# Optimization experiments

Measured on AMD Instinct MI355X. Metric: run time of the kernel, lower is better.

The kernel has to match this reference:

```python
import jax, jax.numpy as jnp
import numpy as np

B, S, H = 2, 8192, 1024
NUM_HEADS = 16
HEAD_DIM = H // NUM_HEADS
KERNEL = 7
DILATION = 1
SCALE = 1.0 / np.sqrt(HEAD_DIM)


def setup_inputs() -> dict:
    key = jax.random.key(0)
    ks = jax.random.split(key, 9)
    init = 0.02
    return {
        "hidden_states": jax.random.normal(ks[0], (B, S, H), dtype=jnp.float32),
        "w_q": jax.random.normal(ks[1], (H, H), dtype=jnp.float32) * init,
        "b_q": jnp.zeros((H,), dtype=jnp.float32),
        "w_k": jax.random.normal(ks[2], (H, H), dtype=jnp.float32) * init,
        "b_k": jnp.zeros((H,), dtype=jnp.float32),
        "w_v": jax.random.normal(ks[3], (H, H), dtype=jnp.float32) * init,
        "b_v": jnp.zeros((H,), dtype=jnp.float32),
        "w_o": jax.random.normal(ks[4], (H, H), dtype=jnp.float32) * init,
        "b_o": jnp.zeros((H,), dtype=jnp.float32),
    }


def reference(hidden_states, w_q, b_q, w_k, b_k, w_v, b_v, w_o, b_o):
    b, s, h = hidden_states.shape
    # QKV projections (weights stored [in, out])
    q = hidden_states @ w_q + b_q
    k = hidden_states @ w_k + b_k
    v = hidden_states @ w_v + b_v
    # [B, nH, S, hd]
    q = q.reshape(b, s, NUM_HEADS, HEAD_DIM).transpose(0, 2, 1, 3)
    k = k.reshape(b, s, NUM_HEADS, HEAD_DIM).transpose(0, 2, 1, 3)
    v = v.reshape(b, s, NUM_HEADS, HEAD_DIM).transpose(0, 2, 1, 3)

    # Neighborhood window indices: for query i, keys at i + (j - K//2)*dilation
    offsets = (jnp.arange(KERNEL) - KERNEL // 2) * DILATION  # [K]
    idx = jnp.arange(s)[:, None] + offsets[None, :]          # [S, K]
    valid = (idx >= 0) & (idx < s)                           # [S, K]
    idx_c = jnp.clip(idx, 0, s - 1)

    k_win = k[:, :, idx_c, :]  # [B, nH, S, K, hd]
    v_win = v[:, :, idx_c, :]  # [B, nH, S, K, hd]

    scores = jnp.einsum('bhsd,bhskd->bhsk', q, k_win) * SCALE
    scores = jnp.where(valid[None, None], scores, -jnp.inf)
    attn = jax.nn.softmax(scores, axis=-1)                   # [B, nH, S, K]
    out = jnp.einsum('bhsk,bhskd->bhsd', attn, v_win)        # [B, nH, S, hd]

    out = out.transpose(0, 2, 1, 3).reshape(b, s, h)
    return out @ w_o + b_o
```

## Files before the change

### kernel.cpp

```cpp
#include <hip/hip_runtime.h>


typedef __bf16 bf16x8 __attribute__((ext_vector_type(8)));
typedef float f32x4 __attribute__((ext_vector_type(4)));
typedef int int4v __attribute__((ext_vector_type(4)));
typedef unsigned short u16x8 __attribute__((ext_vector_type(8)));
typedef __attribute__((address_space(1))) void as1_void;
typedef __attribute__((address_space(3))) void as3_void;

__device__ __forceinline__ float bf2f(unsigned short u) {
    union { unsigned int u; float f; } c;
    c.u = ((unsigned int)u) << 16;
    return c.f;
}
__device__ __forceinline__ unsigned short f2bf(float f) {
    union { float f; unsigned int u; } c;
    c.f = f;
    unsigned int u = c.u;
    u += 0x7fffu + ((u >> 16) & 1u);
    return (unsigned short)(u >> 16);
}

__global__ __launch_bounds__(256) void prep(
    const float* __restrict__ X, const float* __restrict__ w0,
    const float* __restrict__ w1, const float* __restrict__ w2,
    const float* __restrict__ w3, const float* __restrict__ bq,
    const float* __restrict__ bk, const float* __restrict__ bv,
    unsigned short* __restrict__ Xb, unsigned short* __restrict__ t0,
    unsigned short* __restrict__ t3, float* __restrict__ biasQ) {
    __shared__ unsigned short tile[32][33];
    const int bid = blockIdx.x;
    if (bid < 16384) {
        int i = bid * 256 + threadIdx.x;
        float4 v = ((const float4*)X)[i];
        ushort4 o;
        o.x = f2bf(v.x); o.y = f2bf(v.y); o.z = f2bf(v.z); o.w = f2bf(v.w);
        ((ushort4*)Xb)[i] = o;
    } else if (bid < 20480) {
        const int t = bid - 16384;
        const int z = t >> 10;
        const int rem = t & 1023;
        const float* W = (z == 0) ? w0 : (z == 1) ? w1 : (z == 2) ? w2 : w3;
        unsigned short* Wt = (z == 3) ? t3 : t0 + (size_t)z * 1048576;
        const int c0 = (rem & 31) * 32;
        const int r0 = (rem >> 5) * 32;
        const int tx = threadIdx.x & 31;
        const int ty = threadIdx.x >> 5;
#pragma unroll
        for (int i = 0; i < 32; i += 8)
            tile[ty + i][tx] = f2bf(W[(size_t)(r0 + ty + i) * 1024 + c0 + tx]);
        __syncthreads();
#pragma unroll
        for (int i = 0; i < 32; i += 8)
            Wt[(size_t)(c0 + ty + i) * 1024 + r0 + tx] = tile[tx][ty + i];
    } else {
        int i = (bid - 20480) * 256 + threadIdx.x;
        if (i < 3072)
            biasQ[i] = (i < 1024) ? bq[i] : ((i < 2048) ? bk[i - 1024] : bv[i - 2048]);
    }
}

__global__ __launch_bounds__(512, 2) void gemm_qkv8(
    const unsigned short* __restrict__ A, const unsigned short* __restrict__ Bt,
    const float* __restrict__ bias, unsigned short* __restrict__ Cb) {
    constexpr int K = 1024;
    constexpr int NT = 16;
    __shared__ unsigned short smem[65536];
    const int tid  = threadIdx.x;
    const int lane = tid & 63;
    const int wave = tid >> 6;
    const int quad = lane >> 4;
    const int mr   = lane & 15;

    const int id  = blockIdx.x;
    const int swz = (id & 7) * 96 + (id >> 3);
    const int bm  = (swz / 12) * 256;
    const int bn  = (swz % 12) * 256;
    const int wm  = (wave >> 2) * 128;
    const int wn  = (wave & 3) * 64;

    const int r0 = tid >> 3;
    const int g8 = ((lane & 7) ^ ((lane >> 3) & 7)) * 8;
    const unsigned short* srcA = A  + (size_t)(bm + r0) * K + g8;
    const unsigned short* srcB = Bt + (size_t)(bn + r0) * K + g8;

    auto stage = [&](const unsigned short* gb, int ldsByte, int kt) {
#pragma unroll
        for (int l = 0; l < 2; ++l)
            __builtin_amdgcn_global_load_lds(
                (const as1_void*)(gb + (size_t)l * 65536 + kt),
                (as3_void*)((char*)smem + ldsByte + l * 8192 + tid * 16),
                16, 0, 0);
    };

    stage(srcA,          0,     0);
    stage(srcA + 131072, 16384, 0);
    stage(srcB,          32768, 0);
    stage(srcB + 131072, 49152, 0);
    stage(srcB,          65536 + 32768, 64);
    stage(srcB + 131072, 65536 + 49152, 64);
    asm volatile("s_waitcnt vmcnt(4)" ::: "memory");
    asm volatile("s_barrier" ::: "memory");

    const int aRow = (wm + mr) * 64;
    const int bRow = 16384 + (wn + mr) * 64;
    const int c8_0 = ((0 * 4 + quad) ^ (mr & 7)) * 8;
    const int c8_1 = ((1 * 4 + quad) ^ (mr & 7)) * 8;

    f32x4 acc[8][4] = {};

    for (int t = 0; t < NT; ++t) {
        const int bufS  = (t & 1) << 15;
        const int nbufB = ((t + 1) & 1) << 16;
        const int cbufB = (t & 1) << 16;
        const int ktA = (t + 1 < NT ? t + 1 : NT - 1) * 64;
        const int ktB = (t + 2 < NT ? t + 2 : NT - 1) * 64;

        bf16x8 afL[4][2], bA[2][2], bB[2][2];
#pragma unroll
        for (int i = 0; i < 4; ++i) {
            afL[i][0] = *(const bf16x8*)(smem + bufS + aRow + i * 1024 + c8_0);
            afL[i][1] = *(const bf16x8*)(smem + bufS + aRow + i * 1024 + c8_1);
        }
#pragma unroll
        for (int j = 0; j < 2; ++j) {
            bA[j][0] = *(const bf16x8*)(smem + bufS + bRow + j * 1024 + c8_0);
            bA[j][1] = *(const bf16x8*)(smem + bufS + bRow + j * 1024 + c8_1);
        }
#pragma unroll
        for (int j = 0; j < 2; ++j) {
            bB[j][0] = *(const bf16x8*)(smem + bufS + bRow + (j + 2) * 1024 + c8_0);
            bB[j][1] = *(const bf16x8*)(smem + bufS + bRow + (j + 2) * 1024 + c8_1);
        }
        stage(srcA, nbufB, ktA);
        __builtin_amdgcn_s_setprio(1);
#pragma unroll
        for (int i = 0; i < 4; ++i)
#pragma unroll
            for (int j = 0; j < 2; ++j) {
                acc[i][j] = __builtin_amdgcn_mfma_f32_16x16x32_bf16(afL[i][0], bA[j][0], acc[i][j], 0, 0, 0);
                acc[i][j] = __builtin_amdgcn_mfma_f32_16x16x32_bf16(afL[i][1], bA[j][1], acc[i][j], 0, 0, 0);
            }
        __builtin_amdgcn_s_setprio(0);
        asm volatile("s_barrier" ::: "memory");

        stage(srcA + 131072, nbufB + 16384, ktA);
        __builtin_amdgcn_s_setprio(1);
#pragma unroll
        for (int i = 0; i < 4; ++i)
#pragma unroll
            for (int j = 0; j < 2; ++j) {
                acc[i][j + 2] = __builtin_amdgcn_mfma_f32_16x16x32_bf16(afL[i][0], bB[j][0], acc[i][j + 2], 0, 0, 0);
                acc[i][j + 2] = __builtin_amdgcn_mfma_f32_16x16x32_bf16(afL[i][1], bB[j][1], acc[i][j + 2], 0, 0, 0);
            }
        __builtin_amdgcn_s_setprio(0);
        asm volatile("s_barrier" ::: "memory");

        bf16x8 afH[4][2];
#pragma unroll
        for (int i = 0; i < 4; ++i) {
            afH[i][0] = *(const bf16x8*)(smem + bufS + aRow + (i + 4) * 1024 + c8_0);
            afH[i][1] = *(const bf16x8*)(smem + bufS + aRow + (i + 4) * 1024 + c8_1);
        }
        stage(srcB, cbufB + 32768, ktB);
        __builtin_amdgcn_s_setprio(1);
#pragma unroll
        for (int i = 0; i < 4; ++i)
#pragma unroll
            for (int j = 0; j < 2; ++j) {
                acc[i + 4][j + 2] = __builtin_amdgcn_mfma_f32_16x16x32_bf16(afH[i][0], bB[j][0], acc[i + 4][j + 2], 0, 0, 0);
                acc[i + 4][j + 2] = __builtin_amdgcn_mfma_f32_16x16x32_bf16(afH[i][1], bB[j][1], acc[i + 4][j + 2], 0, 0, 0);
            }
        __builtin_amdgcn_s_setprio(0);
        asm volatile("s_barrier" ::: "memory");

        stage(srcB + 131072, cbufB + 49152, ktB);
        __builtin_amdgcn_s_setprio(1);
#pragma unroll
        for (int i = 0; i < 4; ++i)
#pragma unroll
            for (int j = 0; j < 2; ++j) {
                acc[i + 4][j] = __builtin_amdgcn_mfma_f32_16x16x32_bf16(afH[i][0], bA[j][0], acc[i + 4][j], 0, 0, 0);
                acc[i + 4][j] = __builtin_amdgcn_mfma_f32_16x16x32_bf16(afH[i][1], bA[j][1], acc[i + 4][j], 0, 0, 0);
            }
        __builtin_amdgcn_s_setprio(0);
        asm volatile("s_waitcnt vmcnt(4)" ::: "memory");
        asm volatile("s_barrier" ::: "memory");
    }

    asm volatile("s_waitcnt vmcnt(0) lgkmcnt(0)" ::: "memory");
    asm volatile("s_barrier" ::: "memory");

    unsigned short* ep = smem + wave * 8192;
#pragma unroll
    for (int h = 0; h < 2; ++h) {
#pragma unroll
        for (int j = 0; j < 4; ++j) {
            const float bvv = bias[bn + wn + j * 16 + mr];
#pragma unroll
            for (int i = 0; i < 4; ++i)
#pragma unroll
                for (int r = 0; r < 4; ++r)
                    ep[(i * 16 + quad * 4 + r) * 68 + j * 16 + mr] =
                        f2bf(acc[h * 4 + i][j][r] + bvv);
        }
#pragma unroll
        for (int p = 0; p < 8; ++p) {
            const int row = p * 8 + (lane >> 3);
            const int gr = lane & 7;
            int4v v = *(const int4v*)(ep + row * 68 + gr * 8);
            *(int4v*)(Cb + (size_t)(bm + wm + h * 64 + row) * 3072 + bn + wn + gr * 8) = v;
        }
    }
}

__global__ __launch_bounds__(256) void attn_valu(
    const unsigned short* __restrict__ QKV, unsigned short* __restrict__ out) {
    const int tid = threadIdx.x;
    const int h   = tid & 15;
    const int tl  = tid >> 4;
    const int tok = blockIdx.x * 16 + tl;
    const int s   = tok & 8191;
    const size_t base = (size_t)tok * 3072 + h * 64;

    float qf[64];
#pragma unroll
    for (int i = 0; i < 8; ++i) {
        u16x8 qv = *(const u16x8*)(QKV + base + i * 8);
#pragma unroll
        for (int e = 0; e < 8; ++e) qf[i * 8 + e] = bf2f(qv[e]);
    }

    float sc[7];
#pragma unroll
    for (int j = 0; j < 7; ++j) {
        const int ks = s + j - 3;
        const bool ok = (ks >= 0) & (ks < 8192);
        const int kc = ks < 0 ? 0 : (ks > 8191 ? 8191 : ks);
        const size_t kb = base + (size_t)(kc - s) * 3072 + 1024;
        float acc = 0.f;
#pragma unroll
        for (int i = 0; i < 8; ++i) {
            u16x8 kv = *(const u16x8*)(QKV + kb + i * 8);
#pragma unroll
            for (int e = 0; e < 8; ++e) acc += qf[i * 8 + e] * bf2f(kv[e]);
        }
        sc[j] = ok ? acc * 0.125f : -__builtin_inff();
    }

    float mx = sc[0];
#pragma unroll
    for (int j = 1; j < 7; ++j) mx = fmaxf(mx, sc[j]);
    float p[7], sum = 0.f;
#pragma unroll
    for (int j = 0; j < 7; ++j) {
        p[j] = __builtin_amdgcn_exp2f((sc[j] - mx) * 1.44269504f);
        sum += p[j];
    }
    const float inv = __builtin_amdgcn_rcpf(sum);

    float o[64] = {};
#pragma unroll
    for (int j = 0; j < 7; ++j) {
        const int ks = s + j - 3;
        const int kc = ks < 0 ? 0 : (ks > 8191 ? 8191 : ks);
        const size_t vb = base + (size_t)(kc - s) * 3072 + 2048;
        const float pj = p[j] * inv;
#pragma unroll
        for (int i = 0; i < 8; ++i) {
            u16x8 vv = *(const u16x8*)(QKV + vb + i * 8);
#pragma unroll
            for (int e = 0; e < 8; ++e) o[i * 8 + e] += pj * bf2f(vv[e]);
        }
    }

    const size_t dst = (size_t)tok * 1024 + h * 64;
#pragma unroll
    for (int i = 0; i < 8; ++i) {
        u16x8 ov;
#pragma unroll
        for (int e = 0; e < 8; ++e) ov[e] = f2bf(o[i * 8 + e]);
        *(u16x8*)(out + dst + i * 8) = ov;
    }
}

template <int MODE, int MT>
__device__ __forceinline__ void gemm_body(
    const unsigned short* __restrict__ A, const unsigned short* __restrict__ Bt,
    const float* __restrict__ bias, float* __restrict__ Cf,
    int N, int K) {
    __shared__ unsigned short smem[MT * 2048 + 8192];
    const int tid = threadIdx.x;
    const int lane = tid & 63;
    const int wave = tid >> 6;
    const int bm = blockIdx.y * (MT * 32);
    const int bn = blockIdx.x * 128;
    const int wm = (wave >> 1) * (MT * 16);
    const int wn = (wave & 1) * 64;
    const int quad = lane >> 4;
    const int mr = lane & 15;

    const unsigned short* gA[MT];
    const unsigned short* gB[4];
    char* lA[MT];
    char* lB[4];
#pragma unroll
    for (int k = 0; k < MT; ++k) {
        const int q = (k * 4 + wave) * 64 + lane;
        const int row = q >> 3;
        const int c8 = (q & 7) ^ (row & 7);
        gA[k] = A + (size_t)(bm + row) * K + c8 * 8;
        lA[k] = (char*)smem + (size_t)(k * 4 + wave) * 1024;
    }
#pragma unroll
    for (int k = 0; k < 4; ++k) {
        const int q = (k * 4 + wave) * 64 + lane;
        const int row = q >> 3;
        const int c8 = (q & 7) ^ (row & 7);
        gB[k] = Bt + (size_t)(bn + row) * K + c8 * 8;
        lB[k] = (char*)smem + (size_t)MT * 4096 + (size_t)(k * 4 + wave) * 1024;
    }

    f32x4 acc[MT][4] = {};

    for (int kt = 0; kt < K; kt += 64) {
#pragma unroll
        for (int k = 0; k < MT; ++k) {
            __builtin_amdgcn_global_load_lds((as1_void*)gA[k], (as3_void*)lA[k], 16, 0, 0);
            gA[k] += 64;
        }
#pragma unroll
        for (int k = 0; k < 4; ++k) {
            __builtin_amdgcn_global_load_lds((as1_void*)gB[k], (as3_void*)lB[k], 16, 0, 0);
            gB[k] += 64;
        }
        __syncthreads();

#pragma unroll
        for (int kk = 0; kk < 2; ++kk) {
            const int c8 = (kk * 4 + quad) ^ (mr & 7);
            bf16x8 af[MT], bfr[4];
#pragma unroll
            for (int i = 0; i < MT; ++i)
                af[i] = *(const bf16x8*)(smem + (wm + i * 16 + mr) * 64 + c8 * 8);
#pragma unroll
            for (int j = 0; j < 4; ++j)
                bfr[j] = *(const bf16x8*)(smem + MT * 2048 + (wn + j * 16 + mr) * 64 + c8 * 8);
#pragma unroll
            for (int i = 0; i < MT; ++i)
#pragma unroll
                for (int j = 0; j < 4; ++j)
                    acc[i][j] = __builtin_amdgcn_mfma_f32_16x16x32_bf16(
                        af[i], bfr[j], acc[i][j], 0, 0, 0);
        }
        __syncthreads();
    }

    if (MODE == 0) {
        float* epf = (float*)smem + wave * 1280;
#pragma unroll
        for (int j = 0; j < 4; ++j) {
            const int gcol0 = bn + wn + j * 16;
            const float bv = bias[gcol0 + mr];
#pragma unroll
            for (int h2 = 0; h2 < MT / 4; ++h2) {
#pragma unroll
                for (int i2 = 0; i2 < 4; ++i2)
#pragma unroll
                    for (int r = 0; r < 4; ++r)
                        epf[(i2 * 16 + quad * 4 + r) * 20 + mr] = acc[h2 * 4 + i2][j][r] + bv;
#pragma unroll
                for (int p = 0; p < 4; ++p) {
                    const int dr = p * 16 + (lane >> 2);
                    const int ch = lane & 3;
                    f32x4 v = *(const f32x4*)(epf + dr * 20 + ch * 4);
                    *(f32x4*)(Cf + (size_t)(bm + wm + h2 * 64 + dr) * N + gcol0 + ch * 4) = v;
                }
            }
        }
    }
}

__global__ __launch_bounds__(256, 4) void gemm_out(
    const unsigned short* __restrict__ A, const unsigned short* __restrict__ Bt,
    const float* __restrict__ bias, float* __restrict__ Cf, int N, int K) {
    gemm_body<0, 4>(A, Bt, bias, Cf, N, K);
}

extern "C" void kernel_launch(void* const* d_in, const int* in_sizes, int n_in,
                              void* d_out, int out_size, void* d_ws, size_t ws_size,
                              hipStream_t stream) {
    (void)in_sizes; (void)n_in; (void)out_size; (void)ws_size;
    const float* X  = (const float*)d_in[0];
    const float* wq = (const float*)d_in[1];
    const float* bq = (const float*)d_in[2];
    const float* wk = (const float*)d_in[3];
    const float* bk = (const float*)d_in[4];
    const float* wv = (const float*)d_in[5];
    const float* bv = (const float*)d_in[6];
    const float* wo = (const float*)d_in[7];
    const float* bo = (const float*)d_in[8];
    float* out = (float*)d_out;

    char* ws = (char*)d_ws;
    unsigned short* Xb    = (unsigned short*)(ws);
    unsigned short* WtQKV = (unsigned short*)(ws + 33554432);
    unsigned short* WtO   = (unsigned short*)(ws + 39845888);
    unsigned short* QKV   = (unsigned short*)(ws + 41943040);
    unsigned short* AttnO = (unsigned short*)(ws + 142606336);
    float*          biasQ = (float*)(ws + 176160768);

    prep<<<20492, 256, 0, stream>>>(X, wq, wk, wv, wo, bq, bk, bv,
                                    Xb, WtQKV, WtO, biasQ);

    gemm_qkv8<<<768, 512, 0, stream>>>(Xb, WtQKV, biasQ, QKV);

    attn_valu<<<1024, 256, 0, stream>>>(QKV, AttnO);

    gemm_out<<<dim3(8, 128), 256, 0, stream>>>(AttnO, WtO, bo, out, 1024, 1024);
}
```

Before: 354.9 us.

## Remap neighborhood attention to one wave per token with shuffle-reduced dot products

The attention kernel now gives each wavefront one token: each lane holds 8 contiguous elements in each of two 512-wide halves, and the per-head dot products are reduced across 8 lanes with xor shuffles. Before, one thread handled a whole 64-element head, so it carried large per-thread register arrays and issued strided 16-byte loads. The new mapping makes the loads coalesced across lanes, cuts register pressure and raises the grid from 1024 to 4096 blocks. The costs are three shuffle steps per score and redundant softmax work, since every lane in a head group computes the same softmax.

```diff
diff --git a/kernel.cpp b/kernel.cpp
--- a/kernel.cpp
+++ b/kernel.cpp
@@ -214,74 +214,83 @@
     }
 }
 
-__global__ __launch_bounds__(256) void attn_valu(
+__global__ __launch_bounds__(256) void attn_wave(
     const unsigned short* __restrict__ QKV, unsigned short* __restrict__ out) {
-    const int tid = threadIdx.x;
-    const int h   = tid & 15;
-    const int tl  = tid >> 4;
-    const int tok = blockIdx.x * 16 + tl;
-    const int s   = tok & 8191;
-    const size_t base = (size_t)tok * 3072 + h * 64;
-
-    float qf[64];
-#pragma unroll
-    for (int i = 0; i < 8; ++i) {
-        u16x8 qv = *(const u16x8*)(QKV + base + i * 8);
-#pragma unroll
-        for (int e = 0; e < 8; ++e) qf[i * 8 + e] = bf2f(qv[e]);
-    }
-
-    float sc[7];
+    const int lane = threadIdx.x & 63;
+    const int wv   = threadIdx.x >> 6;
+    const int tok  = blockIdx.x * 4 + wv;
+    const int s    = tok & 8191;
+    const size_t rowQ = (size_t)tok * 3072;
+    const int le8 = lane * 8;
+
+    float qf0[8], qf1[8];
+    {
+        u16x8 a = *(const u16x8*)(QKV + rowQ + le8);
+        u16x8 b = *(const u16x8*)(QKV + rowQ + 512 + le8);
+#pragma unroll
+        for (int e = 0; e < 8; ++e) { qf0[e] = bf2f(a[e]); qf1[e] = bf2f(b[e]); }
+    }
+
+    float sc0[7], sc1[7];
 #pragma unroll
     for (int j = 0; j < 7; ++j) {
         const int ks = s + j - 3;
         const bool ok = (ks >= 0) & (ks < 8192);
         const int kc = ks < 0 ? 0 : (ks > 8191 ? 8191 : ks);
-        const size_t kb = base + (size_t)(kc - s) * 3072 + 1024;
-        float acc = 0.f;
-#pragma unroll
-        for (int i = 0; i < 8; ++i) {
-            u16x8 kv = *(const u16x8*)(QKV + kb + i * 8);
-#pragma unroll
-            for (int e = 0; e < 8; ++e) acc += qf[i * 8 + e] * bf2f(kv[e]);
-        }
-        sc[j] = ok ? acc * 0.125f : -__builtin_inff();
-    }
-
-    float mx = sc[0];
-#pragma unroll
-    for (int j = 1; j < 7; ++j) mx = fmaxf(mx, sc[j]);
-    float p[7], sum = 0.f;
+        const size_t kb = rowQ + (size_t)(kc - s) * 3072 + 1024;
+        u16x8 k0 = *(const u16x8*)(QKV + kb + le8);
+        u16x8 k1 = *(const u16x8*)(QKV + kb + 512 + le8);
+        float d0 = 0.f, d1 = 0.f;
+#pragma unroll
+        for (int e = 0; e < 8; ++e) {
+            d0 += qf0[e] * bf2f(k0[e]);
+            d1 += qf1[e] * bf2f(k1[e]);
+        }
+#pragma unroll
+        for (int off = 1; off <= 4; off <<= 1) {
+            d0 += __shfl_xor(d0, off);
+            d1 += __shfl_xor(d1, off);
+        }
+        sc0[j] = ok ? d0 * 0.125f : -__builtin_inff();
+        sc1[j] = ok ? d1 * 0.125f : -__builtin_inff();
+    }
+
+    float mx0 = sc0[0], mx1 = sc1[0];
+#pragma unroll
+    for (int j = 1; j < 7; ++j) { mx0 = fmaxf(mx0, sc0[j]); mx1 = fmaxf(mx1, sc1[j]); }
+    float p0[7], p1[7], sum0 = 0.f, sum1 = 0.f;
 #pragma unroll
     for (int j = 0; j < 7; ++j) {
-        p[j] = __builtin_amdgcn_exp2f((sc[j] - mx) * 1.44269504f);
-        sum += p[j];
-    }
-    const float inv = __builtin_amdgcn_rcpf(sum);
-
-    float o[64] = {};
+        p0[j] = __builtin_amdgcn_exp2f((sc0[j] - mx0) * 1.44269504f);
+        p1[j] = __builtin_amdgcn_exp2f((sc1[j] - mx1) * 1.44269504f);
+        sum0 += p0[j]; sum1 += p1[j];
+    }
+    const float inv0 = __builtin_amdgcn_rcpf(sum0);
+    const float inv1 = __builtin_amdgcn_rcpf(sum1);
+
+    float o0[8] = {}, o1[8] = {};
 #pragma unroll
     for (int j = 0; j < 7; ++j) {
         const int ks = s + j - 3;
         const int kc = ks < 0 ? 0 : (ks > 8191 ? 8191 : ks);
-        const size_t vb = base + (size_t)(kc - s) * 3072 + 2048;
-        const float pj = p[j] * inv;
-#pragma unroll
-        for (int i = 0; i < 8; ++i) {
-            u16x8 vv = *(const u16x8*)(QKV + vb + i * 8);
-#pragma unroll
-            for (int e = 0; e < 8; ++e) o[i * 8 + e] += pj * bf2f(vv[e]);
-        }
-    }
-
-    const size_t dst = (size_t)tok * 1024 + h * 64;
-#pragma unroll
-    for (int i = 0; i < 8; ++i) {
-        u16x8 ov;
-#pragma unroll
-        for (int e = 0; e < 8; ++e) ov[e] = f2bf(o[i * 8 + e]);
-        *(u16x8*)(out + dst + i * 8) = ov;
-    }
+        const size_t vb = rowQ + (size_t)(kc - s) * 3072 + 2048;
+        u16x8 v0 = *(const u16x8*)(QKV + vb + le8);
+        u16x8 v1 = *(const u16x8*)(QKV + vb + 512 + le8);
+        const float w0 = p0[j] * inv0;
+        const float w1 = p1[j] * inv1;
+#pragma unroll
+        for (int e = 0; e < 8; ++e) {
+            o0[e] += w0 * bf2f(v0[e]);
+            o1[e] += w1 * bf2f(v1[e]);
+        }
+    }
+
+    const size_t dst = (size_t)tok * 1024;
+    u16x8 s0v, s1v;
+#pragma unroll
+    for (int e = 0; e < 8; ++e) { s0v[e] = f2bf(o0[e]); s1v[e] = f2bf(o1[e]); }
+    *(u16x8*)(out + dst + le8) = s0v;
+    *(u16x8*)(out + dst + 512 + le8) = s1v;
 }
 
 template <int MODE, int MT>
@@ -415,7 +424,7 @@
 
     gemm_qkv8<<<768, 512, 0, stream>>>(Xb, WtQKV, biasQ, QKV);
 
-    attn_valu<<<1024, 256, 0, stream>>>(QKV, AttnO);
+    attn_wave<<<4096, 256, 0, stream>>>(QKV, AttnO);
 
     gemm_out<<<dim3(8, 128), 256, 0, stream>>>(AttnO, WtO, bo, out, 1024, 1024);
 }
```

Measured after the change: 326.1 us. 1.09x faster.
